# Kernel tuning notes

Hardware: AMD Instinct MI355X
Metric: run time of the kernel (lower is better)

The kernel has to match this reference:

```python
import jax, jax.numpy as jnp
import numpy as np

DT = 0.042
GAMMA = 2.7
EPSILON = 4.7
T, B, N_INP, N_HID, N_OUT = 512, 256, 128, 512, 10


def setup_inputs() -> dict:
    key = jax.random.key(0)
    k1, k2, k3 = jax.random.split(key, 3)
    fan_in = N_INP + 2 * N_HID  # 1152, matches nn.Linear(n_inp+2*n_hid, n_hid)
    bound = 1.0 / np.sqrt(fan_in)
    x = jax.random.normal(k1, (T, B, N_INP), dtype=jnp.float32)
    W = jax.random.uniform(k2, (fan_in, N_HID), dtype=jnp.float32, minval=-bound, maxval=bound)
    b = jnp.zeros((N_HID,), dtype=jnp.float32)
    bound_o = 1.0 / np.sqrt(N_HID)
    Wout = jax.random.uniform(k3, (N_HID, N_OUT), dtype=jnp.float32, minval=-bound_o, maxval=bound_o)
    bout = jnp.zeros((N_OUT,), dtype=jnp.float32)
    return {"x": x, "W": W, "b": b, "Wout": Wout, "bout": bout}


def reference(x, W, b, Wout, bout):
    # x: [T, B, n_inp]; W: [n_inp+2*n_hid, n_hid]
    Bsz = x.shape[1]
    n_hid = W.shape[1]
    hy0 = jnp.zeros((Bsz, n_hid), dtype=x.dtype)
    hz0 = jnp.zeros((Bsz, n_hid), dtype=x.dtype)

    def step(carry, xt):
        hy, hz = carry
        # concat order matches torch.cat((x, hz, hy), 1)
        inp = jnp.concatenate([xt, hz, hy], axis=1)  # [B, n_inp+2*n_hid]
        pre = jnp.tanh(inp @ W + b)
        hz = hz + DT * (pre - GAMMA * hy - EPSILON * hz)
        hy = hy + DT * hz
        return (hy, hz), None

    (hy, hz), _ = jax.lax.scan(step, (hy0, hz0), x)
    output = hy @ Wout + bout  # [B, n_out]
    return output
```

## Files before the change

### kernel.cpp

```cpp
#include <hip/hip_runtime.h>

#define T_STEPS 512
#define BATCH   256
#define N_INP   128
#define N_HID   512
#define N_OUT   10

#define DT_C     0.042f
#define GAMMA_C  2.7f
#define EPS_C    4.7f

#define NWG        128
#define GROUP_WGS  16
#define WG_THREADS 256

typedef short          s16x8  __attribute__((ext_vector_type(8)));
typedef float          f32x16 __attribute__((ext_vector_type(16)));
typedef float          f32x4  __attribute__((ext_vector_type(4)));
typedef unsigned short u16x4  __attribute__((ext_vector_type(4)));
typedef unsigned long long u64;

__device__ inline unsigned short f2bf(float f) {
  union { float f; unsigned u; } v; v.f = f;
  unsigned r = v.u + 0x7fffu + ((v.u >> 16) & 1u);
  return (unsigned short)(r >> 16);
}
__device__ inline float bf2f(unsigned short h) {
  union { unsigned u; float f; } v; v.u = ((unsigned)h) << 16;
  return v.f;
}

__device__ inline void pub8(unsigned short* p, u16x4 v) {
  union { u16x4 v; u64 q; } u; u.v = v;
  __hip_atomic_store((u64*)p, u.q, __ATOMIC_RELAXED, __HIP_MEMORY_SCOPE_AGENT);
}

template<int CI0, int CNT>
__device__ inline void xpart(const float* xrow, int half8,
                             const s16x8* wxhi, const s16x8* wxlo, f32x16& acc) {
  #pragma unroll
  for (int i = 0; i < CNT; ++i) {
    const float* xp = xrow + (CI0 + i) * 16 + half8;
    f32x4 a0 = *reinterpret_cast<const f32x4*>(xp);
    f32x4 a1 = *reinterpret_cast<const f32x4*>(xp + 4);
    s16x8 ahi, alo;
    #pragma unroll
    for (int j = 0; j < 4; ++j) {
      float f0 = a0[j], f1 = a1[j];
      unsigned short h0 = f2bf(f0), h1 = f2bf(f1);
      ahi[j]     = (short)h0;  ahi[j + 4] = (short)h1;
      alo[j]     = (short)f2bf(f0 - bf2f(h0));
      alo[j + 4] = (short)f2bf(f1 - bf2f(h1));
    }
    acc = __builtin_amdgcn_mfma_f32_32x32x16_bf16(ahi, wxhi[i], acc, 0, 0, 0);
    acc = __builtin_amdgcn_mfma_f32_32x32x16_bf16(ahi, wxlo[i], acc, 0, 0, 0);
    acc = __builtin_amdgcn_mfma_f32_32x32x16_bf16(alo, wxhi[i], acc, 0, 0, 0);
  }
}

__global__ __launch_bounds__(WG_THREADS, 1) void cornn_kernel(
    const float* __restrict__ x, const float* __restrict__ W,
    const float* __restrict__ bias, unsigned short* __restrict__ Hbf,
    float* __restrict__ Hy32, unsigned* __restrict__ flags_ws) {
  const int tid   = threadIdx.x;
  const int lane  = tid & 63;
  const int ks    = tid >> 6;
  const int half  = lane >> 5;
  const int half8 = half << 3;
  const int lcol  = lane & 31;
  const int mi    = blockIdx.x & 7;
  const int ni    = blockIdx.x >> 3;
  const int rowA  = (mi << 5) + lcol;

  unsigned* gflags = flags_ws + mi * 64;

  __shared__ float sC[4][1024];
  __shared__ float sB[32];

  s16x8 whi[16], wlo[16];
  s16x8 wxhi[3], wxlo[3];
  const int wcol = (ni << 5) + lcol;
  const int sb = ks << 4;
  #pragma unroll
  for (int i = 0; i < 16; ++i) {
    const int wr = 128 + (sb + i) * 16 + half8;
    const float* wp = W + (size_t)wr * N_HID + wcol;
    s16x8 hi, lo;
    #pragma unroll
    for (int j = 0; j < 8; ++j) {
      float f = wp[(size_t)j * N_HID];
      unsigned short h = f2bf(f);
      hi[j] = (short)h;
      lo[j] = (short)f2bf(f - bf2f(h));
    }
    whi[i] = hi; wlo[i] = lo;
  }
  if (ks < 3) {
    #pragma unroll
    for (int i = 0; i < 3; ++i) {
      const int wr = (ks * 3 + i) * 16 + half8;
      const float* wp = W + (size_t)wr * N_HID + wcol;
      s16x8 hi, lo;
      #pragma unroll
      for (int j = 0; j < 8; ++j) {
        float f = wp[(size_t)j * N_HID];
        unsigned short h = f2bf(f);
        hi[j] = (short)h;
        lo[j] = (short)f2bf(f - bf2f(h));
      }
      wxhi[i] = hi; wxlo[i] = lo;
    }
  }
  if (tid < 32) sB[tid] = bias[(ni << 5) + tid];

  const int e0   = tid << 2;
  const int rowL = e0 >> 5, c0 = e0 & 31;
  const int rowG = (mi << 5) + rowL;
  const int colG = (ni << 5) + c0;
  f32x4 hz = {0.f, 0.f, 0.f, 0.f};
  f32x4 hy = {0.f, 0.f, 0.f, 0.f};

  const unsigned short* hb[2];
  hb[0] = Hbf + (size_t)rowA * 1024 + (sb << 4) + half8;
  hb[1] = hb[0] + 256 * 1024;
  unsigned short* wz[2];
  unsigned short* wy[2];
  wz[0] = Hbf + (size_t)rowG * 1024 + colG;       wz[1] = wz[0] + 256 * 1024;
  wy[0] = wz[0] + 512;                            wy[1] = wz[1] + 512;

  __syncthreads();

  for (int t = 0; t < T_STEPS; ++t) {
    f32x16 acc = {};

    if (ks < 3) {
      const float* xrow = x + (size_t)t * (BATCH * N_INP) + (size_t)rowA * N_INP;
      if (ks == 0)      xpart<0, 3>(xrow, half8, wxhi, wxlo, acc);
      else if (ks == 1) xpart<3, 3>(xrow, half8, wxhi, wxlo, acc);
      else              xpart<6, 2>(xrow, half8, wxhi, wxlo, acc);
    }

    if (t > 0) {
      const unsigned ep = (unsigned)t;
      const int l = lane & 15;
      for (;;) {
        unsigned v = __hip_atomic_load(&gflags[l], __ATOMIC_RELAXED, __HIP_MEMORY_SCOPE_AGENT);
        if (__ballot((lane >= 16) || (l == ni) || (v >= ep)) == ~0ull) break;
        __builtin_amdgcn_s_sleep(2);
      }

      const unsigned short* hp = hb[t & 1];
      f32x4 hbuf[16];
      asm volatile(
        "global_load_dwordx4 %0, %16, off sc0 sc1\n\t"
        "global_load_dwordx4 %1, %16, off offset:32 sc0 sc1\n\t"
        "global_load_dwordx4 %2, %16, off offset:64 sc0 sc1\n\t"
        "global_load_dwordx4 %3, %16, off offset:96 sc0 sc1\n\t"
        "global_load_dwordx4 %4, %16, off offset:128 sc0 sc1\n\t"
        "global_load_dwordx4 %5, %16, off offset:160 sc0 sc1\n\t"
        "global_load_dwordx4 %6, %16, off offset:192 sc0 sc1\n\t"
        "global_load_dwordx4 %7, %16, off offset:224 sc0 sc1\n\t"
        "global_load_dwordx4 %8, %16, off offset:256 sc0 sc1\n\t"
        "global_load_dwordx4 %9, %16, off offset:288 sc0 sc1\n\t"
        "global_load_dwordx4 %10, %16, off offset:320 sc0 sc1\n\t"
        "global_load_dwordx4 %11, %16, off offset:352 sc0 sc1\n\t"
        "global_load_dwordx4 %12, %16, off offset:384 sc0 sc1\n\t"
        "global_load_dwordx4 %13, %16, off offset:416 sc0 sc1\n\t"
        "global_load_dwordx4 %14, %16, off offset:448 sc0 sc1\n\t"
        "global_load_dwordx4 %15, %16, off offset:480 sc0 sc1\n\t"
        "s_waitcnt vmcnt(0)"
        : "=&v"(hbuf[0]),  "=&v"(hbuf[1]),  "=&v"(hbuf[2]),  "=&v"(hbuf[3]),
          "=&v"(hbuf[4]),  "=&v"(hbuf[5]),  "=&v"(hbuf[6]),  "=&v"(hbuf[7]),
          "=&v"(hbuf[8]),  "=&v"(hbuf[9]),  "=&v"(hbuf[10]), "=&v"(hbuf[11]),
          "=&v"(hbuf[12]), "=&v"(hbuf[13]), "=&v"(hbuf[14]), "=&v"(hbuf[15])
        : "v"(hp)
        : "memory");
      #pragma unroll
      for (int i = 0; i < 16; ++i) {
        union { f32x4 f; s16x8 s; } u; u.f = hbuf[i];
        acc = __builtin_amdgcn_mfma_f32_32x32x16_bf16(u.s, whi[i], acc, 0, 0, 0);
        acc = __builtin_amdgcn_mfma_f32_32x32x16_bf16(u.s, wlo[i], acc, 0, 0, 0);
      }
    }

    #pragma unroll
    for (int r = 0; r < 16; ++r) {
      const int rowL_r = (r & 3) + ((r >> 2) << 3) + (half << 2);
      sC[ks][rowL_r * 32 + lcol] = acc[r];
    }
    __syncthreads();

    {
      f32x4 s = *reinterpret_cast<f32x4*>(&sC[0][e0]);
      s += *reinterpret_cast<f32x4*>(&sC[1][e0]);
      s += *reinterpret_cast<f32x4*>(&sC[2][e0]);
      s += *reinterpret_cast<f32x4*>(&sC[3][e0]);
      u16x4 pz, py;
      #pragma unroll
      for (int j = 0; j < 4; ++j) {
        float pre = tanhf(s[j] + sB[c0 + j]);
        float z = hz[j] + DT_C * (pre - GAMMA_C * hy[j] - EPS_C * hz[j]);
        float y = hy[j] + DT_C * z;
        hz[j] = z; hy[j] = y;
        pz[j] = f2bf(z); py[j] = f2bf(y);
      }
      const int wb = (t & 1) ^ 1;
      pub8(wz[wb], pz);
      pub8(wy[wb], py);
    }
    __syncthreads();
    if (tid == 0)
      __hip_atomic_store(&gflags[ni], (unsigned)t + 1u, __ATOMIC_RELAXED, __HIP_MEMORY_SCOPE_AGENT);
  }

  if (Hy32 != nullptr)
    *reinterpret_cast<f32x4*>(Hy32 + (size_t)rowG * 512 + colG) = hy;
}

__global__ void cornn_out_kernel(const float* __restrict__ Hy32,
                                 const unsigned short* __restrict__ HbfFinal,
                                 const float* __restrict__ Wout,
                                 const float* __restrict__ bout,
                                 float* __restrict__ out) {
  const int b = blockIdx.x;
  const int lane = threadIdx.x;
  float a[N_OUT];
  #pragma unroll
  for (int c = 0; c < N_OUT; ++c) a[c] = 0.f;
  #pragma unroll
  for (int j = 0; j < 8; ++j) {
    const int k = lane + (j << 6);
    const float h = Hy32 ? Hy32[(size_t)b * N_HID + k]
                         : bf2f(HbfFinal[(size_t)b * 1024 + 512 + k]);
    const float* wr = Wout + (size_t)k * N_OUT;
    #pragma unroll
    for (int c = 0; c < N_OUT; ++c) a[c] += h * wr[c];
  }
  #pragma unroll
  for (int c = 0; c < N_OUT; ++c) {
    float v = a[c];
    for (int off = 32; off > 0; off >>= 1) v += __shfl_down(v, off, 64);
    if (lane == 0) out[(size_t)b * N_OUT + c] = v + bout[c];
  }
}

extern "C" void kernel_launch(void* const* d_in, const int* in_sizes, int n_in,
                              void* d_out, int out_size, void* d_ws, size_t ws_size,
                              hipStream_t stream) {
  (void)in_sizes; (void)n_in; (void)out_size;
  const float* x    = (const float*)d_in[0];
  const float* W    = (const float*)d_in[1];
  const float* bias = (const float*)d_in[2];
  const float* Wout = (const float*)d_in[3];
  const float* bout = (const float*)d_in[4];

  char* ws = (char*)d_ws;
  unsigned*       flags = (unsigned*)ws;
  unsigned short* Hbf   = (unsigned short*)(ws + 4096);
  float*          Hy32  = (float*)(ws + 4096 + (size_t)2 * 256 * 1024 * 2);
  const size_t needed = 4096 + (size_t)2 * 256 * 1024 * 2 + (size_t)256 * 512 * 4;
  float* hyPtr = (ws_size >= needed) ? Hy32 : nullptr;

  hipMemsetAsync(flags, 0, 4096, stream);

  cornn_kernel<<<dim3(NWG), dim3(WG_THREADS), 0, stream>>>(x, W, bias, Hbf, hyPtr, flags);

  cornn_out_kernel<<<dim3(BATCH), dim3(64), 0, stream>>>(hyPtr, Hbf, Wout, bout,
                                                         (float*)d_out);
}
```

Measured before the change: 2.367 ms.

## Halve workgroup count with 64-column tiles and 8-wave K split

Reorganizes the persistent recurrent kernel from 128 workgroups of 4 waves to 64 workgroups of 8 waves. Each workgroup now owns a 32x64 output tile, and each wave covers one 128-wide K slice of the hidden state plus one 16-wide slice of the input, with two accumulators. This reduces the number of workgroups taking part in the per-step flag barrier and spreads the input projection across all waves. In exchange, the LDS reduction now sums 8 partials instead of 4, LDS use doubles, and fewer CUs are active.

```diff
diff --git a/kernel.cpp b/kernel.cpp
--- a/kernel.cpp
+++ b/kernel.cpp
@@ -10,9 +10,9 @@
 #define GAMMA_C  2.7f
 #define EPS_C    4.7f
 
-#define NWG        128
-#define GROUP_WGS  16
-#define WG_THREADS 256
+#define NWG        64
+#define GROUP_WGS  8
+#define WG_THREADS 512
 
 typedef short          s16x8  __attribute__((ext_vector_type(8)));
 typedef float          f32x16 __attribute__((ext_vector_type(16)));
@@ -35,30 +35,23 @@
   __hip_atomic_store((u64*)p, u.q, __ATOMIC_RELAXED, __HIP_MEMORY_SCOPE_AGENT);
 }
 
-template<int CI0, int CNT>
-__device__ inline void xpart(const float* xrow, int half8,
-                             const s16x8* wxhi, const s16x8* wxlo, f32x16& acc) {
-  #pragma unroll
-  for (int i = 0; i < CNT; ++i) {
-    const float* xp = xrow + (CI0 + i) * 16 + half8;
-    f32x4 a0 = *reinterpret_cast<const f32x4*>(xp);
-    f32x4 a1 = *reinterpret_cast<const f32x4*>(xp + 4);
-    s16x8 ahi, alo;
-    #pragma unroll
-    for (int j = 0; j < 4; ++j) {
-      float f0 = a0[j], f1 = a1[j];
-      unsigned short h0 = f2bf(f0), h1 = f2bf(f1);
-      ahi[j]     = (short)h0;  ahi[j + 4] = (short)h1;
-      alo[j]     = (short)f2bf(f0 - bf2f(h0));
-      alo[j + 4] = (short)f2bf(f1 - bf2f(h1));
-    }
-    acc = __builtin_amdgcn_mfma_f32_32x32x16_bf16(ahi, wxhi[i], acc, 0, 0, 0);
-    acc = __builtin_amdgcn_mfma_f32_32x32x16_bf16(ahi, wxlo[i], acc, 0, 0, 0);
-    acc = __builtin_amdgcn_mfma_f32_32x32x16_bf16(alo, wxhi[i], acc, 0, 0, 0);
-  }
-}
-
-__global__ __launch_bounds__(WG_THREADS, 1) void cornn_kernel(
+#define STATE_LD8(HB, HP)                                                    \
+  asm volatile(                                                              \
+    "global_load_dwordx4 %0, %8, off sc0 sc1\n\t"                            \
+    "global_load_dwordx4 %1, %8, off offset:32 sc0 sc1\n\t"                  \
+    "global_load_dwordx4 %2, %8, off offset:64 sc0 sc1\n\t"                  \
+    "global_load_dwordx4 %3, %8, off offset:96 sc0 sc1\n\t"                  \
+    "global_load_dwordx4 %4, %8, off offset:128 sc0 sc1\n\t"                 \
+    "global_load_dwordx4 %5, %8, off offset:160 sc0 sc1\n\t"                 \
+    "global_load_dwordx4 %6, %8, off offset:192 sc0 sc1\n\t"                 \
+    "global_load_dwordx4 %7, %8, off offset:224 sc0 sc1\n\t"                 \
+    "s_waitcnt vmcnt(0)"                                                     \
+    : "=&v"(HB[0]), "=&v"(HB[1]), "=&v"(HB[2]), "=&v"(HB[3]),                \
+      "=&v"(HB[4]), "=&v"(HB[5]), "=&v"(HB[6]), "=&v"(HB[7])                 \
+    : "v"(HP)                                                                \
+    : "memory")
+
+__global__ __launch_bounds__(WG_THREADS, 2) void cornn_kernel(
     const float* __restrict__ x, const float* __restrict__ W,
     const float* __restrict__ bias, unsigned short* __restrict__ Hbf,
     float* __restrict__ Hy32, unsigned* __restrict__ flags_ws) {
@@ -74,55 +67,54 @@
 
   unsigned* gflags = flags_ws + mi * 64;
 
-  __shared__ float sC[4][1024];
-  __shared__ float sB[32];
-
-  s16x8 whi[16], wlo[16];
-  s16x8 wxhi[3], wxlo[3];
-  const int wcol = (ni << 5) + lcol;
-  const int sb = ks << 4;
-  #pragma unroll
-  for (int i = 0; i < 16; ++i) {
-    const int wr = 128 + (sb + i) * 16 + half8;
-    const float* wp = W + (size_t)wr * N_HID + wcol;
-    s16x8 hi, lo;
+  __shared__ float sC[8][2048];
+  __shared__ float sB[64];
+
+  s16x8 whi0[8], wlo0[8], whi1[8], wlo1[8];
+  s16x8 wxhi0, wxlo0, wxhi1, wxlo1;
+  const int c0t = (ni << 6) + lcol;
+  const int c1t = c0t + 32;
+  #pragma unroll
+  for (int i = 0; i < 8; ++i) {
+    const int wr = 128 + (ks << 7) + i * 16 + half8;
+    const float* wp0 = W + (size_t)wr * N_HID + c0t;
+    s16x8 hi0, lo0, hi1, lo1;
     #pragma unroll
     for (int j = 0; j < 8; ++j) {
-      float f = wp[(size_t)j * N_HID];
-      unsigned short h = f2bf(f);
-      hi[j] = (short)h;
-      lo[j] = (short)f2bf(f - bf2f(h));
-    }
-    whi[i] = hi; wlo[i] = lo;
-  }
-  if (ks < 3) {
-    #pragma unroll
-    for (int i = 0; i < 3; ++i) {
-      const int wr = (ks * 3 + i) * 16 + half8;
-      const float* wp = W + (size_t)wr * N_HID + wcol;
-      s16x8 hi, lo;
-      #pragma unroll
-      for (int j = 0; j < 8; ++j) {
-        float f = wp[(size_t)j * N_HID];
-        unsigned short h = f2bf(f);
-        hi[j] = (short)h;
-        lo[j] = (short)f2bf(f - bf2f(h));
-      }
-      wxhi[i] = hi; wxlo[i] = lo;
-    }
-  }
-  if (tid < 32) sB[tid] = bias[(ni << 5) + tid];
+      float f0 = wp0[(size_t)j * N_HID];
+      float f1 = wp0[(size_t)j * N_HID + 32];
+      unsigned short h0 = f2bf(f0), h1 = f2bf(f1);
+      hi0[j] = (short)h0;  lo0[j] = (short)f2bf(f0 - bf2f(h0));
+      hi1[j] = (short)h1;  lo1[j] = (short)f2bf(f1 - bf2f(h1));
+    }
+    whi0[i] = hi0; wlo0[i] = lo0; whi1[i] = hi1; wlo1[i] = lo1;
+  }
+  {
+    const int wr = (ks << 4) + half8;
+    const float* wp0 = W + (size_t)wr * N_HID + c0t;
+    s16x8 hi0, lo0, hi1, lo1;
+    #pragma unroll
+    for (int j = 0; j < 8; ++j) {
+      float f0 = wp0[(size_t)j * N_HID];
+      float f1 = wp0[(size_t)j * N_HID + 32];
+      unsigned short h0 = f2bf(f0), h1 = f2bf(f1);
+      hi0[j] = (short)h0;  lo0[j] = (short)f2bf(f0 - bf2f(h0));
+      hi1[j] = (short)h1;  lo1[j] = (short)f2bf(f1 - bf2f(h1));
+    }
+    wxhi0 = hi0; wxlo0 = lo0; wxhi1 = hi1; wxlo1 = lo1;
+  }
+  if (tid < 64) sB[tid] = bias[(ni << 6) + tid];
 
   const int e0   = tid << 2;
-  const int rowL = e0 >> 5, c0 = e0 & 31;
+  const int rowL = e0 >> 6, c0 = e0 & 63;
   const int rowG = (mi << 5) + rowL;
-  const int colG = (ni << 5) + c0;
+  const int colG = (ni << 6) + c0;
   f32x4 hz = {0.f, 0.f, 0.f, 0.f};
   f32x4 hy = {0.f, 0.f, 0.f, 0.f};
 
-  const unsigned short* hb[2];
-  hb[0] = Hbf + (size_t)rowA * 1024 + (sb << 4) + half8;
-  hb[1] = hb[0] + 256 * 1024;
+  const unsigned short* hb2[2];
+  hb2[0] = Hbf + (size_t)rowA * 1024 + (ks << 7) + half8;
+  hb2[1] = hb2[0] + 256 * 1024;
   unsigned short* wz[2];
   unsigned short* wy[2];
   wz[0] = Hbf + (size_t)rowG * 1024 + colG;       wz[1] = wz[0] + 256 * 1024;
@@ -131,70 +123,65 @@
   __syncthreads();
 
   for (int t = 0; t < T_STEPS; ++t) {
-    f32x16 acc = {};
-
-    if (ks < 3) {
-      const float* xrow = x + (size_t)t * (BATCH * N_INP) + (size_t)rowA * N_INP;
-      if (ks == 0)      xpart<0, 3>(xrow, half8, wxhi, wxlo, acc);
-      else if (ks == 1) xpart<3, 3>(xrow, half8, wxhi, wxlo, acc);
-      else              xpart<6, 2>(xrow, half8, wxhi, wxlo, acc);
+    f32x16 acc0 = {};
+    f32x16 acc1 = {};
+
+    {
+      const float* xp = x + (size_t)t * (BATCH * N_INP) + (size_t)rowA * N_INP
+                        + (ks << 4) + half8;
+      f32x4 a0 = *reinterpret_cast<const f32x4*>(xp);
+      f32x4 a1 = *reinterpret_cast<const f32x4*>(xp + 4);
+      s16x8 ahi, alo;
+      #pragma unroll
+      for (int j = 0; j < 4; ++j) {
+        float f0 = a0[j], f1 = a1[j];
+        unsigned short h0 = f2bf(f0), h1 = f2bf(f1);
+        ahi[j]     = (short)h0;  ahi[j + 4] = (short)h1;
+        alo[j]     = (short)f2bf(f0 - bf2f(h0));
+        alo[j + 4] = (short)f2bf(f1 - bf2f(h1));
+      }
+      acc0 = __builtin_amdgcn_mfma_f32_32x32x16_bf16(ahi, wxhi0, acc0, 0, 0, 0);
+      acc0 = __builtin_amdgcn_mfma_f32_32x32x16_bf16(ahi, wxlo0, acc0, 0, 0, 0);
+      acc0 = __builtin_amdgcn_mfma_f32_32x32x16_bf16(alo, wxhi0, acc0, 0, 0, 0);
+      acc1 = __builtin_amdgcn_mfma_f32_32x32x16_bf16(ahi, wxhi1, acc1, 0, 0, 0);
+      acc1 = __builtin_amdgcn_mfma_f32_32x32x16_bf16(ahi, wxlo1, acc1, 0, 0, 0);
+      acc1 = __builtin_amdgcn_mfma_f32_32x32x16_bf16(alo, wxhi1, acc1, 0, 0, 0);
     }
 
     if (t > 0) {
       const unsigned ep = (unsigned)t;
-      const int l = lane & 15;
+      const int l = lane & 7;
       for (;;) {
         unsigned v = __hip_atomic_load(&gflags[l], __ATOMIC_RELAXED, __HIP_MEMORY_SCOPE_AGENT);
-        if (__ballot((lane >= 16) || (l == ni) || (v >= ep)) == ~0ull) break;
+        if (__ballot((lane >= 8) | (l == ni) | (v >= ep)) == ~0ull) break;
         __builtin_amdgcn_s_sleep(2);
       }
 
-      const unsigned short* hp = hb[t & 1];
-      f32x4 hbuf[16];
-      asm volatile(
-        "global_load_dwordx4 %0, %16, off sc0 sc1\n\t"
-        "global_load_dwordx4 %1, %16, off offset:32 sc0 sc1\n\t"
-        "global_load_dwordx4 %2, %16, off offset:64 sc0 sc1\n\t"
-        "global_load_dwordx4 %3, %16, off offset:96 sc0 sc1\n\t"
-        "global_load_dwordx4 %4, %16, off offset:128 sc0 sc1\n\t"
-        "global_load_dwordx4 %5, %16, off offset:160 sc0 sc1\n\t"
-        "global_load_dwordx4 %6, %16, off offset:192 sc0 sc1\n\t"
-        "global_load_dwordx4 %7, %16, off offset:224 sc0 sc1\n\t"
-        "global_load_dwordx4 %8, %16, off offset:256 sc0 sc1\n\t"
-        "global_load_dwordx4 %9, %16, off offset:288 sc0 sc1\n\t"
-        "global_load_dwordx4 %10, %16, off offset:320 sc0 sc1\n\t"
-        "global_load_dwordx4 %11, %16, off offset:352 sc0 sc1\n\t"
-        "global_load_dwordx4 %12, %16, off offset:384 sc0 sc1\n\t"
-        "global_load_dwordx4 %13, %16, off offset:416 sc0 sc1\n\t"
-        "global_load_dwordx4 %14, %16, off offset:448 sc0 sc1\n\t"
-        "global_load_dwordx4 %15, %16, off offset:480 sc0 sc1\n\t"
-        "s_waitcnt vmcnt(0)"
-        : "=&v"(hbuf[0]),  "=&v"(hbuf[1]),  "=&v"(hbuf[2]),  "=&v"(hbuf[3]),
-          "=&v"(hbuf[4]),  "=&v"(hbuf[5]),  "=&v"(hbuf[6]),  "=&v"(hbuf[7]),
-          "=&v"(hbuf[8]),  "=&v"(hbuf[9]),  "=&v"(hbuf[10]), "=&v"(hbuf[11]),
-          "=&v"(hbuf[12]), "=&v"(hbuf[13]), "=&v"(hbuf[14]), "=&v"(hbuf[15])
-        : "v"(hp)
-        : "memory");
-      #pragma unroll
-      for (int i = 0; i < 16; ++i) {
+      const unsigned short* hp = hb2[t & 1];
+      f32x4 hbuf[8];
+      STATE_LD8(hbuf, hp);
+      #pragma unroll
+      for (int i = 0; i < 8; ++i) {
         union { f32x4 f; s16x8 s; } u; u.f = hbuf[i];
-        acc = __builtin_amdgcn_mfma_f32_32x32x16_bf16(u.s, whi[i], acc, 0, 0, 0);
-        acc = __builtin_amdgcn_mfma_f32_32x32x16_bf16(u.s, wlo[i], acc, 0, 0, 0);
+        acc0 = __builtin_amdgcn_mfma_f32_32x32x16_bf16(u.s, whi0[i], acc0, 0, 0, 0);
+        acc0 = __builtin_amdgcn_mfma_f32_32x32x16_bf16(u.s, wlo0[i], acc0, 0, 0, 0);
+        acc1 = __builtin_amdgcn_mfma_f32_32x32x16_bf16(u.s, whi1[i], acc1, 0, 0, 0);
+        acc1 = __builtin_amdgcn_mfma_f32_32x32x16_bf16(u.s, wlo1[i], acc1, 0, 0, 0);
       }
     }
 
     #pragma unroll
     for (int r = 0; r < 16; ++r) {
       const int rowL_r = (r & 3) + ((r >> 2) << 3) + (half << 2);
-      sC[ks][rowL_r * 32 + lcol] = acc[r];
+      sC[ks][rowL_r * 64 + lcol]      = acc0[r];
+      sC[ks][rowL_r * 64 + 32 + lcol] = acc1[r];
     }
     __syncthreads();
 
     {
       f32x4 s = *reinterpret_cast<f32x4*>(&sC[0][e0]);
-      s += *reinterpret_cast<f32x4*>(&sC[1][e0]);
-      s += *reinterpret_cast<f32x4*>(&sC[2][e0]);
-      s += *reinterpret_cast<f32x4*>(&sC[3][e0]);
+      #pragma unroll
+      for (int w = 1; w < 8; ++w) s += *reinterpret_cast<f32x4*>(&sC[w][e0]);
       u16x4 pz, py;
       #pragma unroll
       for (int j = 0; j < 4; ++j) {
```

New measurement: 2.285 ms. -3.5%, faster.
